# Kernel optimization log

Measured on AMD Instinct MI355X. Metric: run time of the kernel, lower is better.

## Reference

```python
import jax, jax.numpy as jnp
import numpy as np

NQ = 8          # qubits -> 2^8 = 256 amplitudes
B = 32768       # batch

# ---- gate matrices (torchquantum conventions) ----

def _rx(t):
    c = jnp.cos(t / 2).astype(jnp.complex64)
    s = jnp.sin(t / 2).astype(jnp.complex64)
    return jnp.stack([jnp.stack([c, -1j * s]), jnp.stack([-1j * s, c])])

def _ry(t):
    c = jnp.cos(t / 2).astype(jnp.complex64)
    s = jnp.sin(t / 2).astype(jnp.complex64)
    return jnp.stack([jnp.stack([c, -s]), jnp.stack([s, c])])

def _rz(t):
    tc = t.astype(jnp.complex64)
    z = jnp.zeros((), jnp.complex64)
    return jnp.stack([jnp.stack([jnp.exp(-0.5j * tc), z]),
                      jnp.stack([z, jnp.exp(0.5j * tc)])])

def _u3(p):
    th, ph, lm = p[0], p[1], p[2]
    ct = jnp.cos(th / 2).astype(jnp.complex64)
    st = jnp.sin(th / 2).astype(jnp.complex64)
    eip = jnp.exp(1j * ph.astype(jnp.complex64))
    eil = jnp.exp(1j * lm.astype(jnp.complex64))
    return jnp.stack([jnp.stack([ct, -eil * st]),
                      jnp.stack([eip * st, eip * eil * ct])])

# ---- statevector ops; state shape [B] + [2]*NQ ----

def apply_1q(state, U, w):
    s = jnp.moveaxis(state, 1 + w, -1)
    s = jnp.einsum('ij,b...j->b...i', U, s)
    return jnp.moveaxis(s, -1, 1 + w)

def apply_ctrl(state, U, c, t):
    s = jnp.moveaxis(state, (1 + c, 1 + t), (-2, -1))
    s1 = jnp.einsum('ij,b...j->b...i', U, s[..., 1, :])
    s = jnp.concatenate([s[..., :1, :], s1[..., None, :]], axis=-2)
    return jnp.moveaxis(s, (-2, -1), (1 + c, 1 + t))

def expval_z(state, w):
    p = state.real ** 2 + state.imag ** 2
    axes = tuple(i for i in range(1, NQ + 1) if i != 1 + w)
    pm = jnp.sum(p, axis=axes)  # [B, 2]
    return pm[:, 0] - pm[:, 1]

def encode(x):
    # RY angle encoding: product state, amplitude per qubit = (cos(x/2), sin(x/2))
    a = jnp.stack([jnp.cos(x / 2), jnp.sin(x / 2)], -1).astype(jnp.complex64)  # [B,8,2]
    state = a[:, 0]
    for q in range(1, NQ):
        state = jnp.einsum('b...i,bj->b...ij', state, a[:, q])
    return state  # [B,2,2,...,2]

CR_PAIRS_1 = [(0, 1), (2, 3), (4, 5), (6, 7), (1, 2), (3, 4), (5, 6)]
CR_PAIRS_2 = [(1, 3), (5, 7), (3, 5)]

def branch(state, cr_fn, crp, u3p):
    # crp: [10] angles, u3p: [6,3]
    for i, (c, t) in enumerate(CR_PAIRS_1):
        state = apply_ctrl(state, cr_fn(crp[i]), c, t)
    # intermediate tqm.expval calls do not mutate the state -> omitted
    for i, w in enumerate([1, 3, 5, 7]):
        state = apply_1q(state, _u3(u3p[i]), w)
    for i, (c, t) in enumerate(CR_PAIRS_2):
        state = apply_ctrl(state, cr_fn(crp[7 + i]), c, t)
    state = apply_1q(state, _u3(u3p[4]), 3)
    state = apply_1q(state, _u3(u3p[5]), 7)
    return jnp.stack([expval_z(state, 3), expval_z(state, 7)], axis=1)  # [B,2]


def setup_inputs() -> dict:
    key = jax.random.key(0)
    ks = jax.random.split(key, 12)
    pi = np.float32(np.pi)
    u = lambda k, shape: jax.random.uniform(k, shape, jnp.float32, -pi, pi)
    return {
        'x': u(ks[0], (B, NQ)),
        'crx_params': u(ks[1], (10,)),
        'u3x_params': u(ks[2], (6, 3)),
        'cry_params': u(ks[3], (10,)),
        'u3y_params': u(ks[4], (6, 3)),
        'crz_params': u(ks[5], (10,)),
        'u3z_params': u(ks[6], (6, 3)),
        'w1': jax.random.normal(ks[7], (12, 6), jnp.float32) * 0.3,
        'b1': jnp.zeros((12,), jnp.float32),
        'w2': jax.random.normal(ks[8], (1, 12), jnp.float32) * 0.3,
        'b2': jnp.zeros((1,), jnp.float32),
    }


def reference(x, crx_params, u3x_params, cry_params, u3y_params,
              crz_params, u3z_params, w1, b1, w2, b2):
    state = encode(x)
    fx = branch(state, _rx, crx_params, u3x_params)  # CRX branch (qdev)
    fy = branch(state, _ry, cry_params, u3y_params)  # CRY branch (qdev1)
    fz = branch(state, _rz, crz_params, u3z_params)  # CRZ branch (qdev2)
    feats = jnp.concatenate([fx, fy, fz], axis=1)    # [B,6]
    h = jnp.tanh(feats @ w1.T + b1)
    return jax.nn.sigmoid(h @ w2.T + b2)             # [B,1]
```

## Files before the change

### kernel.cpp

```cpp
#include <hip/hip_runtime.h>
#include <math.h>


typedef float v2f __attribute__((ext_vector_type(2)));

__device__ __forceinline__ v2f mk2(float a, float b) { v2f r; r.x = a; r.y = b; return r; }
__device__ __forceinline__ v2f ld2(const float* __restrict__ p) { return *(const v2f*)p; }

__device__ __forceinline__ v2f pk_mul_s(v2f a, v2f b) { v2f d;
  asm("v_pk_mul_f32 %0, %1, %2 op_sel:[0,0] op_sel_hi:[0,1]" : "=v"(d) : "v"(a), "v"(b)); return d; }
__device__ __forceinline__ v2f pk_fma_irot(v2f a, v2f b, v2f c) { v2f d;
  asm("v_pk_fma_f32 %0, %1, %2, %3 op_sel:[1,1,0] op_sel_hi:[1,0,1] neg_lo:[0,1,0]" : "=v"(d) : "v"(a), "v"(b), "v"(c)); return d; }
__device__ __forceinline__ v2f cmul(v2f a, v2f b) { return pk_fma_irot(a, b, pk_mul_s(a, b)); }
__device__ __forceinline__ v2f pk_mul_swap(v2f a, v2f b) { v2f d;
  asm("v_pk_mul_f32 %0, %1, %2 op_sel:[1,0] op_sel_hi:[0,1]" : "=v"(d) : "v"(a), "v"(b)); return d; }

__device__ __forceinline__ v2f pk_mul_sM(v2f M, v2f b) { v2f d;
  asm("v_pk_mul_f32 %0, %1, %2 op_sel:[0,0] op_sel_hi:[0,1]" : "=v"(d) : "s"(M), "v"(b)); return d; }
__device__ __forceinline__ v2f pk_fma_sloM(v2f M, v2f b, v2f c) { v2f d;
  asm("v_pk_fma_f32 %0, %1, %2, %3 op_sel:[0,0,0] op_sel_hi:[0,1,1]" : "=v"(d) : "s"(M), "v"(b), "v"(c)); return d; }
__device__ __forceinline__ v2f pk_fma_shiM(v2f M, v2f b, v2f c) { v2f d;
  asm("v_pk_fma_f32 %0, %1, %2, %3 op_sel:[1,0,0] op_sel_hi:[1,1,1]" : "=v"(d) : "s"(M), "v"(b), "v"(c)); return d; }
__device__ __forceinline__ v2f pk_fma_shi_negM(v2f M, v2f b, v2f c) { v2f d;
  asm("v_pk_fma_f32 %0, %1, %2, %3 op_sel:[1,0,0] op_sel_hi:[1,1,1] neg_lo:[1,0,0] neg_hi:[1,0,0]" : "=v"(d) : "s"(M), "v"(b), "v"(c)); return d; }
__device__ __forceinline__ v2f pk_fma_rotM(v2f M, v2f b, v2f c) { v2f d;
  asm("v_pk_fma_f32 %0, %1, %2, %3 op_sel:[1,1,0] op_sel_hi:[1,0,1] neg_hi:[0,1,0]" : "=v"(d) : "s"(M), "v"(b), "v"(c)); return d; }
__device__ __forceinline__ v2f pk_fma_irotM(v2f M, v2f b, v2f c) { v2f d;
  asm("v_pk_fma_f32 %0, %1, %2, %3 op_sel:[1,1,0] op_sel_hi:[1,0,1] neg_lo:[0,1,0]" : "=v"(d) : "s"(M), "v"(b), "v"(c)); return d; }

template <int MASK>
__device__ __forceinline__ float swz1(float v) {
  constexpr int pat = (MASK << 10) | 0x1F;
  return __int_as_float(__builtin_amdgcn_ds_swizzle(__float_as_int(v), pat));
}
template <int MASK>
__device__ __forceinline__ v2f swz2(v2f v) {
  v2f r; r.x = swz1<MASK>(v.x); r.y = swz1<MASK>(v.y); return r;
}

template <bool A_REAL>
__device__ __forceinline__ v2f u3row_s(v2f ua, v2f ub, v2f a, v2f b) {
  v2f t = pk_mul_sM(ua, a);
  if constexpr (!A_REAL) t = pk_fma_irotM(ua, a, t);
  t = pk_fma_sloM(ub, b, t);
  return pk_fma_irotM(ub, b, t);
}

template <int SB>
__device__ __forceinline__ void u3_apply(v2f w[32], const float* __restrict__ p) {
  const v2f M0 = ld2(p), M1 = ld2(p + 2), M2 = ld2(p + 4), M3 = ld2(p + 6);
#pragma unroll
  for (int i = 0; i < 32; ++i) {
    if (i & (1 << SB)) continue;
    const int i1 = i | (1 << SB);
    const v2f a = w[i], b = w[i1];
    w[i] = u3row_s<true>(M0, M1, a, b);
    w[i1] = u3row_s<false>(M3, M2, b, a);
  }
}

template <int SB, int CB, bool M00R>
__device__ __forceinline__ void u3_sel(v2f w[32], const float* __restrict__ pM,
                                       const float* __restrict__ pN) {
  const v2f M0 = ld2(pM), M1 = ld2(pM + 2), M2 = ld2(pM + 4), M3 = ld2(pM + 6);
  const v2f N0 = ld2(pN), N1 = ld2(pN + 2), N2 = ld2(pN + 4), N3 = ld2(pN + 6);
#pragma unroll
  for (int i = 0; i < 32; ++i) {
    if (i & (1 << SB)) continue;
    const int i1 = i | (1 << SB);
    const v2f a = w[i], b = w[i1];
    if ((i >> CB) & 1) {
      w[i] = u3row_s<false>(N0, N1, a, b);
      w[i1] = u3row_s<false>(N3, N2, b, a);
    } else {
      w[i] = u3row_s<M00R>(M0, M1, a, b);
      w[i1] = u3row_s<false>(M3, M2, b, a);
    }
  }
}

template <int SB, int LB>
__device__ __forceinline__ void crx_Sc_Lt(v2f w[32], v2f cs) {
#pragma unroll
  for (int i = 0; i < 32; ++i) {
    if (!(i & (1 << SB))) continue;
    const v2f p = swz2<(1 << LB)>(w[i]);
    w[i] = pk_fma_rotM(cs, p, pk_mul_sM(cs, w[i]));
  }
}

template <int SB, int LB>
__device__ __forceinline__ void cr_ry_r(float w[32], v2f cs, int gl) {
  const bool tb = (gl >> LB) & 1;
  const float Ky = tb ? cs.y : -cs.y;
#pragma unroll
  for (int i = 0; i < 32; ++i) {
    if (!(i & (1 << SB))) continue;
    const float p = swz1<(1 << LB)>(w[i]);
    w[i] = __builtin_fmaf(Ky, p, cs.x * w[i]);
  }
}

template <int KIND, int SBc, int SBt>
__device__ __forceinline__ void cr_Sc_St(v2f w[32], v2f cs) {
#pragma unroll
  for (int i = 0; i < 32; ++i) {
    if (!(i & (1 << SBc))) continue;
    if constexpr (KIND == 2) {
      const v2f t = pk_mul_sM(cs, w[i]);
      w[i] = (i & (1 << SBt)) ? pk_fma_irotM(cs, w[i], t)
                              : pk_fma_rotM(cs, w[i], t);
    } else {
      if (i & (1 << SBt)) continue;
      const int i1 = i | (1 << SBt);
      const v2f a = w[i], b = w[i1];
      if constexpr (KIND == 0) {
        w[i] = pk_fma_rotM(cs, b, pk_mul_sM(cs, a));
        w[i1] = pk_fma_rotM(cs, a, pk_mul_sM(cs, b));
      } else {
        w[i] = pk_fma_shi_negM(cs, b, pk_mul_sM(cs, a));
        w[i1] = pk_fma_shiM(cs, a, pk_mul_sM(cs, b));
      }
    }
  }
}

template <int SB>
__device__ __forceinline__ void u3_lift(v2f w[32], const float wr[32],
                                        const float* __restrict__ p) {
  const v2f M0 = ld2(p), M1 = ld2(p + 2), M2 = ld2(p + 4), M3 = ld2(p + 6);
#pragma unroll
  for (int i = 0; i < 32; ++i) {
    if (i & (1 << SB)) continue;
    const int i1 = i | (1 << SB);
    const float a = wr[i], b = wr[i1];
    w[i] = mk2(__builtin_fmaf(a, M0.x, b * M1.x), b * M1.y);
    w[i1] = mk2(__builtin_fmaf(a, M2.x, b * M3.x),
                __builtin_fmaf(a, M2.y, b * M3.y));
  }
}

__device__ __forceinline__ void measure2(v2f w[32], const float* __restrict__ q,
                                         v2f res[2]) {
  const v2f qa = ld2(q);
  const v2f qg = ld2(q + 2);
  float z3[2], z7[2];
#pragma unroll
  for (int e = 0; e < 2; ++e) {
    float z3a = 0.f, z3b = 0.f, z7p = 0.f, z7m = 0.f;
#pragma unroll
    for (int s0 = 0; s0 < 16; s0 += 2) {
      const v2f a = w[e * 16 + s0], b = w[e * 16 + s0 + 1];
      const v2f t1 = a * b, t2 = pk_mul_swap(a, b), t3 = a * a, t4 = b * b;
      const float r = t1.x + t1.y;
      const float m = t2.x - t2.y;
      const float na = t3.x + t3.y;
      const float nb = t4.x + t4.y;
      z3a = __builtin_fmaf(qa.x, na, z3a);
      z3b = __builtin_fmaf(qa.y, nb, z3b);
      z3a = __builtin_fmaf(qg.x, r, z3a);
      z3b = __builtin_fmaf(-qg.y, m, z3b);
      const float nn = na + nb;
      if (s0 & 2) z7m += nn; else z7p += nn;
    }
    z3[e] = z3a + z3b;
    z7[e] = z7p - z7m;
  }
  z3[0] += swz1<1>(z3[0]); z3[1] += swz1<1>(z3[1]); z7[0] += swz1<1>(z7[0]); z7[1] += swz1<1>(z7[1]);
  z3[0] += swz1<2>(z3[0]); z3[1] += swz1<2>(z3[1]); z7[0] += swz1<2>(z7[0]); z7[1] += swz1<2>(z7[1]);
  z3[0] += swz1<4>(z3[0]); z3[1] += swz1<4>(z3[1]); z7[0] += swz1<4>(z7[0]); z7[1] += swz1<4>(z7[1]);
  z3[0] += swz1<8>(z3[0]); z3[1] += swz1<8>(z3[1]); z7[0] += swz1<8>(z7[0]); z7[1] += swz1<8>(z7[1]);
  res[0] = mk2(z3[0], z7[0]);
  res[1] = mk2(z3[1], z7[1]);
}

template <int KIND>
__device__ __forceinline__ void tail_common(v2f w[32], const float* __restrict__ Gb,
                                            v2f res[2]) {
  u3_sel<0, 3, true>(w, Gb + 72, Gb + 80);
  u3_apply<2>(w, Gb + 88);
  u3_sel<1, 2, false>(w, Gb + 96, Gb + 104);
  cr_Sc_St<KIND, 0, 2>(w, ld2(Gb + 56));
  measure2(w, Gb + 112, res);
}

__device__ __forceinline__ void load_sincos(const float* __restrict__ xb,
                                            float sn[8], float cn[8]) {
  const float4 xlo = ((const float4*)xb)[0];
  const float4 xhi = ((const float4*)xb)[1];
  const float xq[8] = {xlo.x, xlo.y, xlo.z, xlo.w, xhi.x, xhi.y, xhi.z, xhi.w};
#pragma unroll
  for (int q = 0; q < 8; ++q) __sincosf(0.5f * xq[q], &sn[q], &cn[q]);
}

__device__ __forceinline__ void run_rx(const float* __restrict__ xb0,
                                       const float* __restrict__ xb1,
                                       const float* __restrict__ Gb, int gl,
                                       v2f res[2]) {
  const bool l0 = gl & 1, l1 = (gl >> 1) & 1, l2 = (gl >> 2) & 1, l3 = (gl >> 3) & 1;
  v2f w[32];
#pragma unroll
  for (int e = 0; e < 2; ++e) {
    float sn[8], cn[8];
    load_sincos(e ? xb1 : xb0, sn, cn);
    v2f pa[4], pb[4];
#pragma unroll
    for (int pr = 0; pr < 4; ++pr) {
      const bool lh = (pr == 0) ? l0 : (pr == 1) ? l1 : (pr == 2) ? l2 : l3;
      const float c = Gb[pr * 8], s = Gb[pr * 8 + 1];
      const float uc = lh ? sn[2 * pr] : cn[2 * pr];
      const float b0 = uc * cn[2 * pr + 1], b1 = uc * sn[2 * pr + 1];
      const float Kx = lh ? c : 1.f;
      const float Kyn = lh ? -s : 0.f;
      pa[pr] = mk2(Kx * b0, Kyn * b1);
      pb[pr] = mk2(Kx * b1, Kyn * b0);
    }
    v2f A[4] = {cmul(pa[0], pa[2]), cmul(pa[0], pb[2]), cmul(pb[0], pa[2]), cmul(pb[0], pb[2])};
    v2f Bv[4] = {cmul(pa[3], pa[1]), cmul(pa[3], pb[1]), cmul(pb[3], pa[1]), cmul(pb[3], pb[1])};
#pragma unroll
    for (int s = 0; s < 16; ++s) w[e * 16 + s] = cmul(A[s >> 2], Bv[s & 3]);
  }
  crx_Sc_Lt<3, 1>(w, ld2(Gb + 32));
  crx_Sc_Lt<0, 2>(w, ld2(Gb + 40));
  crx_Sc_Lt<2, 3>(w, ld2(Gb + 48));
  u3_apply<3>(w, Gb + 64);
  tail_common<0>(w, Gb, res);
}

__device__ __forceinline__ void run_ry(const float* __restrict__ xb0,
                                       const float* __restrict__ xb1,
                                       const float* __restrict__ Gb, int gl,
                                       v2f res[2]) {
  const bool l0 = gl & 1, l1 = (gl >> 1) & 1, l2 = (gl >> 2) & 1, l3 = (gl >> 3) & 1;
  float wr[32];
#pragma unroll
  for (int e = 0; e < 2; ++e) {
    float sn[8], cn[8];
    load_sincos(e ? xb1 : xb0, sn, cn);
    float pa[4], pb[4];
#pragma unroll
    for (int pr = 0; pr < 4; ++pr) {
      const bool lh = (pr == 0) ? l0 : (pr == 1) ? l1 : (pr == 2) ? l2 : l3;
      const float c = Gb[pr * 8], s = Gb[pr * 8 + 1];
      const float uc = lh ? sn[2 * pr] : cn[2 * pr];
      const float b0 = uc * cn[2 * pr + 1], b1 = uc * sn[2 * pr + 1];
      const float Kx = lh ? c : 1.f;
      const float Ky = lh ? s : 0.f;
      pa[pr] = Kx * b0 - Ky * b1;
      pb[pr] = Ky * b0 + Kx * b1;
    }
    const float A[4] = {pa[0] * pa[2], pa[0] * pb[2], pb[0] * pa[2], pb[0] * pb[2]};
    const float Bv[4] = {pa[3] * pa[1], pa[3] * pb[1], pb[3] * pa[1], pb[3] * pb[1]};
#pragma unroll
    for (int s = 0; s < 16; ++s) wr[e * 16 + s] = A[s >> 2] * Bv[s & 3];
  }
  cr_ry_r<3, 1>(wr, ld2(Gb + 32), gl);
  cr_ry_r<0, 2>(wr, ld2(Gb + 40), gl);
  cr_ry_r<2, 3>(wr, ld2(Gb + 48), gl);
  v2f w[32];
  u3_lift<3>(w, wr, Gb + 64);
  tail_common<1>(w, Gb, res);
}

__device__ __forceinline__ void run_rz(const float* __restrict__ xb0,
                                       const float* __restrict__ xb1,
                                       const float* __restrict__ Gb, int gl,
                                       v2f res[2]) {
  const bool l0 = gl & 1, l1 = (gl >> 1) & 1, l2 = (gl >> 2) & 1, l3 = (gl >> 3) & 1;
  const float t0 = Gb[2], h0 = Gb[3];
  const float t1 = Gb[10], h1 = Gb[11];
  const float t2 = Gb[18], h2 = Gb[19];
  const float t3 = Gb[26], h3 = Gb[27];
  const float h4 = Gb[35], h5 = Gb[43], h6 = Gb[51];
  const float kk0 = (l1 ? t1 : 0.f) + (l2 ? h5 : -h5);
  const float kk1 = (l3 ? t3 : 0.f);
  const float kk2 = (l2 ? t2 : 0.f) + (l3 ? h6 : -h6);
  const float kk3 = (l0 ? t0 : 0.f) + (l1 ? h4 : -h4);
  const float aa = -((l0 ? h0 : 0.f) + (l1 ? h1 : 0.f) + (l2 ? h2 : 0.f) + (l3 ? h3 : 0.f));
  float v01[2][4], v23[2][4];
#pragma unroll
  for (int e = 0; e < 2; ++e) {
    float sn[8], cn[8];
    load_sincos(e ? xb1 : xb0, sn, cn);
    const float u0 = l0 ? sn[0] : cn[0];
    const float u2 = l1 ? sn[2] : cn[2];
    const float u4 = l2 ? sn[4] : cn[4];
    const float u6 = l3 ? sn[6] : cn[6];
    const float P = (u0 * u2) * (u4 * u6);
    v01[e][0] = P * (cn[3] * cn[7]); v01[e][1] = P * (sn[3] * cn[7]);
    v01[e][2] = P * (cn[3] * sn[7]); v01[e][3] = P * (sn[3] * sn[7]);
    v23[e][0] = cn[5] * cn[1]; v23[e][1] = sn[5] * cn[1];
    v23[e][2] = cn[5] * sn[1]; v23[e][3] = sn[5] * sn[1];
  }
  v2f w[32];
#pragma unroll
  for (int s = 0; s < 16; ++s) {
    float phv = aa;
    if (s & 1) phv += kk0;
    if (s & 2) phv += kk1;
    if (s & 4) phv += kk2;
    if (s & 8) phv += kk3;
    float sp, cp;
    __sincosf(phv, &sp, &cp);
    const float e0 = v01[0][s & 3] * v23[0][s >> 2];
    const float e1 = v01[1][s & 3] * v23[1][s >> 2];
    w[s] = mk2(e0 * cp, e0 * sp);
    w[16 + s] = mk2(e1 * cp, e1 * sp);
  }
  u3_apply<3>(w, Gb + 64);
  tail_common<2>(w, Gb, res);
}

struct c2 { float r, i; };
__device__ __forceinline__ c2 cmulh(c2 a, c2 b) { return {a.r * b.r - a.i * b.i, a.r * b.i + a.i * b.r}; }
__device__ __forceinline__ c2 cmulc(c2 a, c2 b) { return {a.r * b.r + a.i * b.i, a.i * b.r - a.r * b.i}; }
__device__ __forceinline__ c2 caddh(c2 a, c2 b) { return {a.r + b.r, a.i + b.i}; }
__device__ void mat2mul(const c2 A[4], const c2 B[4], c2 C[4]) {
  C[0] = caddh(cmulh(A[0], B[0]), cmulh(A[1], B[2]));
  C[1] = caddh(cmulh(A[0], B[1]), cmulh(A[1], B[3]));
  C[2] = caddh(cmulh(A[2], B[0]), cmulh(A[3], B[2]));
  C[3] = caddh(cmulh(A[2], B[1]), cmulh(A[3], B[3]));
}
__device__ void u3m(const float* p, c2 M[4]) {
  float st, ct, sp, cp, sl, cl;
  sincosf(0.5f * p[0], &st, &ct);
  sincosf(p[1], &sp, &cp);
  sincosf(p[2], &sl, &cl);
  M[0] = {ct, 0.f};
  M[1] = {-cl * st, -sl * st};
  M[2] = {cp * st, sp * st};
  M[3] = {(cp * cl - sp * sl) * ct, (sp * cl + cp * sl) * ct};
}
__device__ void rmat(int kind, float th, c2 R[4]) {
  float s, c;
  sincosf(0.5f * th, &s, &c);
  if (kind == 0) { R[0] = {c, 0.f}; R[1] = {0.f, -s}; R[2] = {0.f, -s}; R[3] = {c, 0.f}; }
  else if (kind == 1) { R[0] = {c, 0.f}; R[1] = {-s, 0.f}; R[2] = {s, 0.f}; R[3] = {c, 0.f}; }
  else { R[0] = {c, -s}; R[1] = {0.f, 0.f}; R[2] = {0.f, 0.f}; R[3] = {c, s}; }
}
__device__ void storeM(float* dst, const c2 M[4]) {
#pragma unroll
  for (int j = 0; j < 4; ++j) { dst[2 * j] = M[j].r; dst[2 * j + 1] = M[j].i; }
}

__global__ void qcnn_prep(const float* __restrict__ crx, const float* __restrict__ u3x,
                          const float* __restrict__ cry, const float* __restrict__ u3y,
                          const float* __restrict__ crz, const float* __restrict__ u3z,
                          float* __restrict__ G) {
  const int br = threadIdx.x;
  if (br >= 3) return;
  const float* crp = (br == 0) ? crx : (br == 1) ? cry : crz;
  const float* u3p = (br == 0) ? u3x : (br == 1) ? u3y : u3z;
  float* Gb = G + br * 128;

  const int crIdx[8] = {0, 1, 2, 3, 4, 5, 6, 9};
#pragma unroll
  for (int i = 0; i < 8; ++i) {
    const float th = crp[crIdx[i]];
    float s, c;
    sincosf(0.5f * th, &s, &c);
    Gb[i * 8] = c;
    Gb[i * 8 + 1] = s;
    Gb[i * 8 + 2] = th;
    Gb[i * 8 + 3] = 0.5f * th;
  }
  c2 U1v[4], U3v[4], U5v[4], U7a[4], U7b[4], U3f[4], R[4], T[4], T2[4];
  u3m(u3p + 0, U1v);
  u3m(u3p + 3, U3v);
  u3m(u3p + 6, U5v);
  u3m(u3p + 9, U7a);
  u3m(u3p + 12, U3f);
  u3m(u3p + 15, U7b);
  storeM(Gb + 64, U1v);
  storeM(Gb + 72, U3v);
  rmat(br, crp[7], R);
  mat2mul(R, U3v, T);
  storeM(Gb + 80, T);
  storeM(Gb + 88, U5v);
  mat2mul(U7b, U7a, T);
  storeM(Gb + 96, T);
  rmat(br, crp[8], R);
  mat2mul(R, U7a, T);
  mat2mul(U7b, T, T2);
  storeM(Gb + 104, T2);
  const float n00 = U3f[0].r * U3f[0].r + U3f[0].i * U3f[0].i;
  const float n01 = U3f[1].r * U3f[1].r + U3f[1].i * U3f[1].i;
  const float n10 = U3f[2].r * U3f[2].r + U3f[2].i * U3f[2].i;
  const float n11 = U3f[3].r * U3f[3].r + U3f[3].i * U3f[3].i;
  const c2 g01 = cmulc(U3f[0], U3f[1]);
  const c2 g23 = cmulc(U3f[2], U3f[3]);
  Gb[112] = n00 - n10;
  Gb[113] = n01 - n11;
  Gb[114] = 2.f * (g01.r - g23.r);
  Gb[115] = 2.f * (g01.i - g23.i);
}

__global__ __launch_bounds__(256) void qcnn_main(
    const float* __restrict__ x, const float* __restrict__ G,
    const float* __restrict__ w1, const float* __restrict__ b1,
    const float* __restrict__ w2, const float* __restrict__ b2,
    float* __restrict__ out, int B) {
  const int gid = blockIdx.x * blockDim.x + threadIdx.x;
  const int grp = gid >> 4;
  const int gl = threadIdx.x & 15;
  const int b0 = grp * 2;
  if (b0 >= B) return;
  const float* xb0 = x + b0 * 8;
  const float* xb1 = x + (b0 + 1) * 8;

  v2f fx[2], fy[2], fz[2];
  run_rx(xb0, xb1, G, gl, fx);
  run_ry(xb0, xb1, G + 128, gl, fy);
  run_rz(xb0, xb1, G + 256, gl, fz);

  const int j = (gl < 12) ? gl : 0;
  const float* w1r = w1 + j * 6;
  const float w10 = w1r[0], w11 = w1r[1], w12 = w1r[2];
  const float w13 = w1r[3], w14 = w1r[4], w15 = w1r[5];
  const float b1v = b1[j], w2v = w2[j], b2v = b2[0];
  float a0 = b1v + w10 * fx[0].x + w11 * fx[0].y + w12 * fy[0].x +
             w13 * fy[0].y + w14 * fz[0].x + w15 * fz[0].y;
  float a1 = b1v + w10 * fx[1].x + w11 * fx[1].y + w12 * fy[1].x +
             w13 * fy[1].y + w14 * fz[1].x + w15 * fz[1].y;
  const float e0 = __expf(2.f * a0), e1 = __expf(2.f * a1);
  const float th0 = 1.f - 2.f * __builtin_amdgcn_rcpf(e0 + 1.f);
  const float th1 = 1.f - 2.f * __builtin_amdgcn_rcpf(e1 + 1.f);
  float t0 = (gl < 12) ? w2v * th0 : 0.f;
  float t1 = (gl < 12) ? w2v * th1 : 0.f;
  t0 += swz1<1>(t0); t1 += swz1<1>(t1);
  t0 += swz1<2>(t0); t1 += swz1<2>(t1);
  t0 += swz1<4>(t0); t1 += swz1<4>(t1);
  t0 += swz1<8>(t0); t1 += swz1<8>(t1);
  const float r0 = __builtin_amdgcn_rcpf(1.f + __expf(-(t0 + b2v)));
  const float r1 = __builtin_amdgcn_rcpf(1.f + __expf(-(t1 + b2v)));
  if (gl == 0) {
    out[b0] = r0;
    out[b0 + 1] = r1;
  }
}

extern "C" void kernel_launch(void* const* d_in, const int* in_sizes, int n_in,
                              void* d_out, int out_size, void* d_ws,
                              size_t ws_size, hipStream_t stream) {
  const float* x = (const float*)d_in[0];
  const float* crx = (const float*)d_in[1];
  const float* u3x = (const float*)d_in[2];
  const float* cry = (const float*)d_in[3];
  const float* u3y = (const float*)d_in[4];
  const float* crz = (const float*)d_in[5];
  const float* u3z = (const float*)d_in[6];
  const float* w1 = (const float*)d_in[7];
  const float* b1 = (const float*)d_in[8];
  const float* w2 = (const float*)d_in[9];
  const float* b2 = (const float*)d_in[10];
  float* out = (float*)d_out;
  float* G = (float*)d_ws;
  const int B = in_sizes[0] / 8;

  hipLaunchKernelGGL(qcnn_prep, dim3(1), dim3(64), 0, stream, crx, u3x, cry,
                     u3y, crz, u3z, G);
  const int ngroups = (B + 1) / 2;
  const int threads = 256;
  const int blocks = (ngroups * 16 + threads - 1) / threads;
  hipLaunchKernelGGL(qcnn_main, dim3(blocks), dim3(threads), 0, stream, x, G,
                     w1, b1, w2, b2, out, B);
}
```

Baseline: 105.2 us.

## Process four batch elements per 16-lane group and use DPP for short shuffles

```diff
diff --git a/kernel.cpp b/kernel.cpp
--- a/kernel.cpp
+++ b/kernel.cpp
@@ -1,6 +1,9 @@
 #include <hip/hip_runtime.h>
 #include <math.h>
 
+
+constexpr int NE = 4;
+constexpr int NW = NE * 16;
 
 typedef float v2f __attribute__((ext_vector_type(2)));
 
@@ -29,13 +32,19 @@
   asm("v_pk_fma_f32 %0, %1, %2, %3 op_sel:[1,1,0] op_sel_hi:[1,0,1] neg_lo:[0,1,0]" : "=v"(d) : "s"(M), "v"(b), "v"(c)); return d; }
 
 template <int MASK>
-__device__ __forceinline__ float swz1(float v) {
-  constexpr int pat = (MASK << 10) | 0x1F;
-  return __int_as_float(__builtin_amdgcn_ds_swizzle(__float_as_int(v), pat));
+__device__ __forceinline__ float shuf1(float v) {
+  if constexpr (MASK == 1) {
+    return __int_as_float(__builtin_amdgcn_mov_dpp(__float_as_int(v), 0xB1, 0xf, 0xf, true));
+  } else if constexpr (MASK == 2) {
+    return __int_as_float(__builtin_amdgcn_mov_dpp(__float_as_int(v), 0x4E, 0xf, 0xf, true));
+  } else {
+    constexpr int pat = (MASK << 10) | 0x1F;
+    return __int_as_float(__builtin_amdgcn_ds_swizzle(__float_as_int(v), pat));
+  }
 }
 template <int MASK>
-__device__ __forceinline__ v2f swz2(v2f v) {
-  v2f r; r.x = swz1<MASK>(v.x); r.y = swz1<MASK>(v.y); return r;
+__device__ __forceinline__ v2f shuf2(v2f v) {
+  v2f r; r.x = shuf1<MASK>(v.x); r.y = shuf1<MASK>(v.y); return r;
 }
 
 template <bool A_REAL>
@@ -47,10 +56,10 @@
 }
 
 template <int SB>
-__device__ __forceinline__ void u3_apply(v2f w[32], const float* __restrict__ p) {
+__device__ __forceinline__ void u3_apply(v2f w[NW], const float* __restrict__ p) {
   const v2f M0 = ld2(p), M1 = ld2(p + 2), M2 = ld2(p + 4), M3 = ld2(p + 6);
 #pragma unroll
-  for (int i = 0; i < 32; ++i) {
+  for (int i = 0; i < NW; ++i) {
     if (i & (1 << SB)) continue;
     const int i1 = i | (1 << SB);
     const v2f a = w[i], b = w[i1];
@@ -60,12 +69,12 @@
 }
 
 template <int SB, int CB, bool M00R>
-__device__ __forceinline__ void u3_sel(v2f w[32], const float* __restrict__ pM,
+__device__ __forceinline__ void u3_sel(v2f w[NW], const float* __restrict__ pM,
                                        const float* __restrict__ pN) {
   const v2f M0 = ld2(pM), M1 = ld2(pM + 2), M2 = ld2(pM + 4), M3 = ld2(pM + 6);
   const v2f N0 = ld2(pN), N1 = ld2(pN + 2), N2 = ld2(pN + 4), N3 = ld2(pN + 6);
 #pragma unroll
-  for (int i = 0; i < 32; ++i) {
+  for (int i = 0; i < NW; ++i) {
     if (i & (1 << SB)) continue;
     const int i1 = i | (1 << SB);
     const v2f a = w[i], b = w[i1];
@@ -80,31 +89,31 @@
 }
 
 template <int SB, int LB>
-__device__ __forceinline__ void crx_Sc_Lt(v2f w[32], v2f cs) {
-#pragma unroll
-  for (int i = 0; i < 32; ++i) {
+__device__ __forceinline__ void crx_Sc_Lt(v2f w[NW], v2f cs) {
+#pragma unroll
+  for (int i = 0; i < NW; ++i) {
     if (!(i & (1 << SB))) continue;
-    const v2f p = swz2<(1 << LB)>(w[i]);
+    const v2f p = shuf2<(1 << LB)>(w[i]);
     w[i] = pk_fma_rotM(cs, p, pk_mul_sM(cs, w[i]));
   }
 }
 
 template <int SB, int LB>
-__device__ __forceinline__ void cr_ry_r(float w[32], v2f cs, int gl) {
+__device__ __forceinline__ void cr_ry_r(float w[NW], v2f cs, int gl) {
   const bool tb = (gl >> LB) & 1;
   const float Ky = tb ? cs.y : -cs.y;
 #pragma unroll
-  for (int i = 0; i < 32; ++i) {
+  for (int i = 0; i < NW; ++i) {
     if (!(i & (1 << SB))) continue;
-    const float p = swz1<(1 << LB)>(w[i]);
+    const float p = shuf1<(1 << LB)>(w[i]);
     w[i] = __builtin_fmaf(Ky, p, cs.x * w[i]);
   }
 }
 
 template <int KIND, int SBc, int SBt>
-__device__ __forceinline__ void cr_Sc_St(v2f w[32], v2f cs) {
-#pragma unroll
-  for (int i = 0; i < 32; ++i) {
+__device__ __forceinline__ void cr_Sc_St(v2f w[NW], v2f cs) {
+#pragma unroll
+  for (int i = 0; i < NW; ++i) {
     if (!(i & (1 << SBc))) continue;
     if constexpr (KIND == 2) {
       const v2f t = pk_mul_sM(cs, w[i]);
@@ -126,11 +135,11 @@
 }
 
 template <int SB>
-__device__ __forceinline__ void u3_lift(v2f w[32], const float wr[32],
+__device__ __forceinline__ void u3_lift(v2f w[NW], const float wr[NW],
                                         const float* __restrict__ p) {
   const v2f M0 = ld2(p), M1 = ld2(p + 2), M2 = ld2(p + 4), M3 = ld2(p + 6);
 #pragma unroll
-  for (int i = 0; i < 32; ++i) {
+  for (int i = 0; i < NW; ++i) {
     if (i & (1 << SB)) continue;
     const int i1 = i | (1 << SB);
     const float a = wr[i], b = wr[i1];
@@ -140,13 +149,13 @@
   }
 }
 
-__device__ __forceinline__ void measure2(v2f w[32], const float* __restrict__ q,
-                                         v2f res[2]) {
+__device__ __forceinline__ void measureN(v2f w[NW], const float* __restrict__ q,
+                                         v2f res[NE]) {
   const v2f qa = ld2(q);
   const v2f qg = ld2(q + 2);
-  float z3[2], z7[2];
-#pragma unroll
-  for (int e = 0; e < 2; ++e) {
+  float z3[NE], z7[NE];
+#pragma unroll
+  for (int e = 0; e < NE; ++e) {
     float z3a = 0.f, z3b = 0.f, z7p = 0.f, z7m = 0.f;
 #pragma unroll
     for (int s0 = 0; s0 < 16; s0 += 2) {
@@ -166,22 +175,24 @@
     z3[e] = z3a + z3b;
     z7[e] = z7p - z7m;
   }
-  z3[0] += swz1<1>(z3[0]); z3[1] += swz1<1>(z3[1]); z7[0] += swz1<1>(z7[0]); z7[1] += swz1<1>(z7[1]);
-  z3[0] += swz1<2>(z3[0]); z3[1] += swz1<2>(z3[1]); z7[0] += swz1<2>(z7[0]); z7[1] += swz1<2>(z7[1]);
-  z3[0] += swz1<4>(z3[0]); z3[1] += swz1<4>(z3[1]); z7[0] += swz1<4>(z7[0]); z7[1] += swz1<4>(z7[1]);
-  z3[0] += swz1<8>(z3[0]); z3[1] += swz1<8>(z3[1]); z7[0] += swz1<8>(z7[0]); z7[1] += swz1<8>(z7[1]);
-  res[0] = mk2(z3[0], z7[0]);
-  res[1] = mk2(z3[1], z7[1]);
+#pragma unroll
+  for (int e = 0; e < NE; ++e) {
+    z3[e] += shuf1<1>(z3[e]); z7[e] += shuf1<1>(z7[e]);
+    z3[e] += shuf1<2>(z3[e]); z7[e] += shuf1<2>(z7[e]);
+    z3[e] += shuf1<4>(z3[e]); z7[e] += shuf1<4>(z7[e]);
+    z3[e] += shuf1<8>(z3[e]); z7[e] += shuf1<8>(z7[e]);
+    res[e] = mk2(z3[e], z7[e]);
+  }
 }
 
 template <int KIND>
-__device__ __forceinline__ void tail_common(v2f w[32], const float* __restrict__ Gb,
-                                            v2f res[2]) {
+__device__ __forceinline__ void tail_common(v2f w[NW], const float* __restrict__ Gb,
+                                            v2f res[NE]) {
   u3_sel<0, 3, true>(w, Gb + 72, Gb + 80);
   u3_apply<2>(w, Gb + 88);
   u3_sel<1, 2, false>(w, Gb + 96, Gb + 104);
   cr_Sc_St<KIND, 0, 2>(w, ld2(Gb + 56));
-  measure2(w, Gb + 112, res);
+  measureN(w, Gb + 112, res);
 }
 
 __device__ __forceinline__ void load_sincos(const float* __restrict__ xb,
@@ -193,27 +204,27 @@
   for (int q = 0; q < 8; ++q) __sincosf(0.5f * xq[q], &sn[q], &cn[q]);
 }
 
-__device__ __forceinline__ void run_rx(const float* __restrict__ xb0,
-                                       const float* __restrict__ xb1,
+__device__ __forceinline__ void run_rx(const float* __restrict__ x, int b0, int B,
                                        const float* __restrict__ Gb, int gl,
-                                       v2f res[2]) {
+                                       v2f res[NE]) {
   const bool l0 = gl & 1, l1 = (gl >> 1) & 1, l2 = (gl >> 2) & 1, l3 = (gl >> 3) & 1;
-  v2f w[32];
-#pragma unroll
-  for (int e = 0; e < 2; ++e) {
+  v2f w[NW];
+#pragma unroll
+  for (int e = 0; e < NE; ++e) {
+    const int b = min(b0 + e, B - 1);
     float sn[8], cn[8];
-    load_sincos(e ? xb1 : xb0, sn, cn);
+    load_sincos(x + b * 8, sn, cn);
     v2f pa[4], pb[4];
 #pragma unroll
     for (int pr = 0; pr < 4; ++pr) {
       const bool lh = (pr == 0) ? l0 : (pr == 1) ? l1 : (pr == 2) ? l2 : l3;
       const float c = Gb[pr * 8], s = Gb[pr * 8 + 1];
       const float uc = lh ? sn[2 * pr] : cn[2 * pr];
-      const float b0 = uc * cn[2 * pr + 1], b1 = uc * sn[2 * pr + 1];
+      const float b0f = uc * cn[2 * pr + 1], b1f = uc * sn[2 * pr + 1];
       const float Kx = lh ? c : 1.f;
       const float Kyn = lh ? -s : 0.f;
-      pa[pr] = mk2(Kx * b0, Kyn * b1);
-      pb[pr] = mk2(Kx * b1, Kyn * b0);
+      pa[pr] = mk2(Kx * b0f, Kyn * b1f);
+      pb[pr] = mk2(Kx * b1f, Kyn * b0f);
     }
     v2f A[4] = {cmul(pa[0], pa[2]), cmul(pa[0], pb[2]), cmul(pb[0], pa[2]), cmul(pb[0], pb[2])};
     v2f Bv[4] = {cmul(pa[3], pa[1]), cmul(pa[3], pb[1]), cmul(pb[3], pa[1]), cmul(pb[3], pb[1])};
@@ -227,27 +238,27 @@
   tail_common<0>(w, Gb, res);
 }
 
-__device__ __forceinline__ void run_ry(const float* __restrict__ xb0,
-                                       const float* __restrict__ xb1,
+__device__ __forceinline__ void run_ry(const float* __restrict__ x, int b0, int B,
                                        const float* __restrict__ Gb, int gl,
-                                       v2f res[2]) {
+                                       v2f res[NE]) {
   const bool l0 = gl & 1, l1 = (gl >> 1) & 1, l2 = (gl >> 2) & 1, l3 = (gl >> 3) & 1;
-  float wr[32];
-#pragma unroll
-  for (int e = 0; e < 2; ++e) {
+  float wr[NW];
+#pragma unroll
+  for (int e = 0; e < NE; ++e) {
+    const int b = min(b0 + e, B - 1);
     float sn[8], cn[8];
-    load_sincos(e ? xb1 : xb0, sn, cn);
+    load_sincos(x + b * 8, sn, cn);
     float pa[4], pb[4];
 #pragma unroll
     for (int pr = 0; pr < 4; ++pr) {
       const bool lh = (pr == 0) ? l0 : (pr == 1) ? l1 : (pr == 2) ? l2 : l3;
       const float c = Gb[pr * 8], s = Gb[pr * 8 + 1];
       const float uc = lh ? sn[2 * pr] : cn[2 * pr];
-      const float b0 = uc * cn[2 * pr + 1], b1 = uc * sn[2 * pr + 1];
+      const float b0f = uc * cn[2 * pr + 1], b1f = uc * sn[2 * pr + 1];
       const float Kx = lh ? c : 1.f;
       const float Ky = lh ? s : 0.f;
-      pa[pr] = Kx * b0 - Ky * b1;
-      pb[pr] = Ky * b0 + Kx * b1;
+      pa[pr] = Kx * b0f - Ky * b1f;
+      pb[pr] = Ky * b0f + Kx * b1f;
     }
     const float A[4] = {pa[0] * pa[2], pa[0] * pb[2], pb[0] * pa[2], pb[0] * pb[2]};
     const float Bv[4] = {pa[3] * pa[1], pa[3] * pb[1], pb[3] * pa[1], pb[3] * pb[1]};
@@ -257,15 +268,14 @@
   cr_ry_r<3, 1>(wr, ld2(Gb + 32), gl);
   cr_ry_r<0, 2>(wr, ld2(Gb + 40), gl);
   cr_ry_r<2, 3>(wr, ld2(Gb + 48), gl);
-  v2f w[32];
+  v2f w[NW];
   u3_lift<3>(w, wr, Gb + 64);
   tail_common<1>(w, Gb, res);
 }
 
-__device__ __forceinline__ void run_rz(const float* __restrict__ xb0,
-                                       const float* __restrict__ xb1,
+__device__ __forceinline__ void run_rz(const float* __restrict__ x, int b0, int B,
                                        const float* __restrict__ Gb, int gl,
-                                       v2f res[2]) {
+                                       v2f res[NE]) {
   const bool l0 = gl & 1, l1 = (gl >> 1) & 1, l2 = (gl >> 2) & 1, l3 = (gl >> 3) & 1;
   const float t0 = Gb[2], h0 = Gb[3];
   const float t1 = Gb[10], h1 = Gb[11];
@@ -277,11 +287,12 @@
   const float kk2 = (l2 ? t2 : 0.f) + (l3 ? h6 : -h6);
   const float kk3 = (l0 ? t0 : 0.f) + (l1 ? h4 : -h4);
   const float aa = -((l0 ? h0 : 0.f) + (l1 ? h1 : 0.f) + (l2 ? h2 : 0.f) + (l3 ? h3 : 0.f));
-  float v01[2][4], v23[2][4];
-#pragma unroll
-  for (int e = 0; e < 2; ++e) {
+  float v01[NE][4], v23[NE][4];
+#pragma unroll
+  for (int e = 0; e < NE; ++e) {
+    const int b = min(b0 + e, B - 1);
     float sn[8], cn[8];
-    load_sincos(e ? xb1 : xb0, sn, cn);
+    load_sincos(x + b * 8, sn, cn);
     const float u0 = l0 ? sn[0] : cn[0];
     const float u2 = l1 ? sn[2] : cn[2];
     const float u4 = l2 ? sn[4] : cn[4];
@@ -292,7 +303,7 @@
     v23[e][0] = cn[5] * cn[1]; v23[e][1] = sn[5] * cn[1];
     v23[e][2] = cn[5] * sn[1]; v23[e][3] = sn[5] * sn[1];
   }
-  v2f w[32];
+  v2f w[NW];
 #pragma unroll
   for (int s = 0; s < 16; ++s) {
     float phv = aa;
@@ -302,10 +313,11 @@
     if (s & 8) phv += kk3;
     float sp, cp;
     __sincosf(phv, &sp, &cp);
-    const float e0 = v01[0][s & 3] * v23[0][s >> 2];
-    const float e1 = v01[1][s & 3] * v23[1][s >> 2];
-    w[s] = mk2(e0 * cp, e0 * sp);
-    w[16 + s] = mk2(e1 * cp, e1 * sp);
+#pragma unroll
+    for (int e = 0; e < NE; ++e) {
+      const float ev = v01[e][s & 3] * v23[e][s >> 2];
+      w[e * 16 + s] = mk2(ev * cp, ev * sp);
+    }
   }
   u3_apply<3>(w, Gb + 64);
   tail_common<2>(w, Gb, res);
@@ -403,39 +415,42 @@
   const int gid = blockIdx.x * blockDim.x + threadIdx.x;
   const int grp = gid >> 4;
   const int gl = threadIdx.x & 15;
-  const int b0 = grp * 2;
+  const int b0 = grp * NE;
   if (b0 >= B) return;
-  const float* xb0 = x + b0 * 8;
-  const float* xb1 = x + (b0 + 1) * 8;
-
-  v2f fx[2], fy[2], fz[2];
-  run_rx(xb0, xb1, G, gl, fx);
-  run_ry(xb0, xb1, G + 128, gl, fy);
-  run_rz(xb0, xb1, G + 256, gl, fz);
+
+  v2f fx[NE], fy[NE], fz[NE];
+  run_rx(x, b0, B, G, gl, fx);
+  run_ry(x, b0, B, G + 128, gl, fy);
+  run_rz(x, b0, B, G + 256, gl, fz);
 
   const int j = (gl < 12) ? gl : 0;
   const float* w1r = w1 + j * 6;
   const float w10 = w1r[0], w11 = w1r[1], w12 = w1r[2];
   const float w13 = w1r[3], w14 = w1r[4], w15 = w1r[5];
   const float b1v = b1[j], w2v = w2[j], b2v = b2[0];
-  float a0 = b1v + w10 * fx[0].x + w11 * fx[0].y + w12 * fy[0].x +
-             w13 * fy[0].y + w14 * fz[0].x + w15 * fz[0].y;
-  float a1 = b1v + w10 * fx[1].x + w11 * fx[1].y + w12 * fy[1].x +
-             w13 * fy[1].y + w14 * fz[1].x + w15 * fz[1].y;
-  const float e0 = __expf(2.f * a0), e1 = __expf(2.f * a1);
-  const float th0 = 1.f - 2.f * __builtin_amdgcn_rcpf(e0 + 1.f);
-  const float th1 = 1.f - 2.f * __builtin_amdgcn_rcpf(e1 + 1.f);
-  float t0 = (gl < 12) ? w2v * th0 : 0.f;
-  float t1 = (gl < 12) ? w2v * th1 : 0.f;
-  t0 += swz1<1>(t0); t1 += swz1<1>(t1);
-  t0 += swz1<2>(t0); t1 += swz1<2>(t1);
-  t0 += swz1<4>(t0); t1 += swz1<4>(t1);
-  t0 += swz1<8>(t0); t1 += swz1<8>(t1);
-  const float r0 = __builtin_amdgcn_rcpf(1.f + __expf(-(t0 + b2v)));
-  const float r1 = __builtin_amdgcn_rcpf(1.f + __expf(-(t1 + b2v)));
+  float t[NE];
+#pragma unroll
+  for (int e = 0; e < NE; ++e) {
+    const float a = b1v + w10 * fx[e].x + w11 * fx[e].y + w12 * fy[e].x +
+                    w13 * fy[e].y + w14 * fz[e].x + w15 * fz[e].y;
+    const float ev = __expf(2.f * a);
+    const float th = 1.f - 2.f * __builtin_amdgcn_rcpf(ev + 1.f);
+    t[e] = (gl < 12) ? w2v * th : 0.f;
+  }
+#pragma unroll
+  for (int e = 0; e < NE; ++e) {
+    t[e] += shuf1<1>(t[e]);
+    t[e] += shuf1<2>(t[e]);
+    t[e] += shuf1<4>(t[e]);
+    t[e] += shuf1<8>(t[e]);
+  }
   if (gl == 0) {
-    out[b0] = r0;
-    out[b0 + 1] = r1;
+#pragma unroll
+    for (int e = 0; e < NE; ++e) {
+      const int b = b0 + e;
+      if (b < B)
+        out[b] = __builtin_amdgcn_rcpf(1.f + __expf(-(t[e] + b2v)));
+    }
   }
 }
 
@@ -459,7 +474,7 @@
 
   hipLaunchKernelGGL(qcnn_prep, dim3(1), dim3(64), 0, stream, crx, u3x, cry,
                      u3y, crz, u3z, G);
-  const int ngroups = (B + 1) / 2;
+  const int ngroups = (B + NE - 1) / NE;
   const int threads = 256;
   const int blocks = (ngroups * 16 + threads - 1) / threads;
   hipLaunchKernelGGL(qcnn_main, dim3(blocks), dim3(threads), 0, stream, x, G,
```

Result: slower. 187.2 us (+78.0%).
